# Kernel tuning notes

Measured on AMD Instinct MI355X. Metric: run time of the kernel, lower is better.

The kernel has to match this reference:

```python
import jax, jax.numpy as jnp
import numpy as np

N, F_IN, HID, H1, NG = 50000, 128, 64, 4, 512
E = 800000


def setup_inputs() -> dict:
    key = jax.random.key(0)
    ks = jax.random.split(key, 16)
    x = jax.random.normal(ks[0], (N, F_IN), dtype=jnp.float32)
    edge_index = jax.random.randint(ks[1], (2, E), 0, N, dtype=jnp.int64)
    batch = jnp.sort(jax.random.randint(ks[2], (N,), 0, NG, dtype=jnp.int64))
    s = 0.05
    W1 = jax.random.normal(ks[3], (F_IN, H1 * HID), dtype=jnp.float32) * s
    a_src1 = jax.random.normal(ks[4], (H1, HID), dtype=jnp.float32) * s
    a_dst1 = jax.random.normal(ks[5], (H1, HID), dtype=jnp.float32) * s
    b1 = jnp.zeros((H1 * HID,), dtype=jnp.float32)
    W2 = jax.random.normal(ks[6], (H1 * HID, HID), dtype=jnp.float32) * s
    a_src2 = jax.random.normal(ks[7], (1, HID), dtype=jnp.float32) * s
    a_dst2 = jax.random.normal(ks[8], (1, HID), dtype=jnp.float32) * s
    b2 = jnp.zeros((HID,), dtype=jnp.float32)
    Wc = jax.random.normal(ks[9], (HID, 2), dtype=jnp.float32) * s
    bc = jnp.zeros((2,), dtype=jnp.float32)
    return dict(x=x, edge_index=edge_index, batch=batch, W1=W1, a_src1=a_src1,
                a_dst1=a_dst1, b1=b1, W2=W2, a_src2=a_src2, a_dst2=a_dst2,
                b2=b2, Wc=Wc, bc=bc)


def gat_layer(x, W, a_src, a_dst, bias, src, dst, n):
    # PyG GATConv: h = x @ W per head; e_ij = LeakyReLU(a_src.h_j + a_dst.h_i),
    # softmax over incoming edges of each dst node, then scatter-add aggregate.
    H, D = a_src.shape
    h = (x @ W).reshape(n, H, D)                       # [N,H,D]
    asrc = jnp.einsum('nhd,hd->nh', h, a_src)          # [N,H]
    adst = jnp.einsum('nhd,hd->nh', h, a_dst)
    e = jax.nn.leaky_relu(asrc[src] + adst[dst], 0.2)  # [E,H]
    m = jax.lax.stop_gradient(jax.ops.segment_max(e, dst, num_segments=n))
    p = jnp.exp(e - m[dst])
    s = jax.ops.segment_sum(p, dst, num_segments=n)
    alpha = p / (s[dst] + 1e-16)                       # [E,H]
    out = jax.ops.segment_sum(alpha[:, :, None] * h[src], dst, num_segments=n)
    return out.reshape(n, H * D) + bias


def reference(x, edge_index, batch, W1, a_src1, a_dst1, b1, W2, a_src2, a_dst2, b2, Wc, bc):
    n = x.shape[0]
    loops = jnp.arange(n, dtype=edge_index.dtype)
    src = jnp.concatenate([edge_index[0], loops])  # add self-loops (PyG default)
    dst = jnp.concatenate([edge_index[1], loops])
    h = jax.nn.relu(gat_layer(x, W1, a_src1, a_dst1, b1, src, dst, n))
    h = jax.nn.relu(gat_layer(h, W2, a_src2, a_dst2, b2, src, dst, n))
    # global mean pool over graphs
    ng = NG
    sums = jax.ops.segment_sum(h, batch, num_segments=ng)
    cnts = jax.ops.segment_sum(jnp.ones((n,), h.dtype), batch, num_segments=ng)
    pooled = sums / jnp.maximum(cnts, 1.0)[:, None]
    logits = pooled @ Wc + bc
    return jax.nn.log_softmax(logits, axis=1)
```

## Files before the change

kernel.cpp:

```cpp
#include <hip/hip_runtime.h>
#include <hip/hip_bf16.h>
#include <cstddef>
#include <cstdint>

#define FIN   128
#define HID   64
#define H1    4
#define NGRAPH 512

typedef short bf16x8 __attribute__((ext_vector_type(8)));
typedef float f32x4  __attribute__((ext_vector_type(4)));

#if defined(__has_builtin)
#if __has_builtin(__builtin_amdgcn_cvt_f32_fp8) && __has_builtin(__builtin_amdgcn_cvt_pk_fp8_f32)
#define HAVE_HW_FP8 1
#endif
#endif

__device__ __forceinline__ float wave_reduce_sum(float v) {
  #pragma unroll
  for (int off = 32; off > 0; off >>= 1) v += __shfl_down(v, off, 64);
  return v;
}

__device__ __forceinline__ float leaky02(float x) {
  return x > 0.0f ? x : 0.2f * x;
}

__device__ __forceinline__ float bf2f(unsigned short u) {
  union { unsigned int i; float f; } v; v.i = ((unsigned int)u) << 16; return v.f;
}
__device__ __forceinline__ unsigned short f2bf(float f) {
  union { float f; unsigned int i; } v; v.f = f;
  unsigned int b = v.i;
  return (unsigned short)((b + 0x7FFFu + ((b >> 16) & 1u)) >> 16);
}

#ifndef HAVE_HW_FP8
__device__ __forceinline__ unsigned char f2fp8_1(float f) {
  unsigned int u = __float_as_uint(f);
  unsigned int s = u >> 31;
  u &= 0x7fffffffu;
  if (u > 0x43e00000u) u = 0x43e00000u;
  unsigned int b = u + (0x0007FFFFu + ((u >> 20) & 1u));
  int e = (int)(b >> 23) - 127;
  unsigned int m = (b >> 20) & 7u;
  unsigned char o;
  if (e < -9) o = 0;
  else if (e < -6) { int sh = -6 - e; o = (unsigned char)((8u | m) >> sh); }
  else if (e > 8) o = 0x7e;
  else o = (unsigned char)(((e + 7) << 3) | m);
  return o | (unsigned char)(s << 7);
}
__device__ __forceinline__ float fp8tof_1(unsigned char b) {
  unsigned int s = b >> 7, e = (b >> 3) & 15u, m = b & 7u;
  float v = (e == 0) ? (float)m * 0.001953125f
                     : (float)(8u + m) * __uint_as_float((117u + e) << 23);
  return s ? -v : v;
}
#endif

__device__ __forceinline__ unsigned char f2fp8(float f) {
#ifdef HAVE_HW_FP8
  return (unsigned char)(__builtin_amdgcn_cvt_pk_fp8_f32(f, f, 0u, false) & 0xffu);
#else
  return f2fp8_1(f);
#endif
}
__device__ __forceinline__ float fp8dec(unsigned int w, int i) {
#ifdef HAVE_HW_FP8
  switch (i) {
    case 0: return __builtin_amdgcn_cvt_f32_fp8(w, 0);
    case 1: return __builtin_amdgcn_cvt_f32_fp8(w, 1);
    case 2: return __builtin_amdgcn_cvt_f32_fp8(w, 2);
    default: return __builtin_amdgcn_cvt_f32_fp8(w, 3);
  }
#else
  return fp8tof_1((unsigned char)((w >> (8 * i)) & 0xffu));
#endif
}

__global__ void pre_kernel(const float* __restrict__ x, const float* __restrict__ W1,
                           const float* __restrict__ W2, unsigned short* __restrict__ xb,
                           unsigned short* __restrict__ W1T, unsigned short* __restrict__ W2T,
                           const int* __restrict__ batch, int* __restrict__ gstart,
                           int* __restrict__ gend, int nx8, int N) {
  int t = blockIdx.x * blockDim.x + threadIdx.x;
  if (t < nx8) {
    const float4* xp = (const float4*)x + (size_t)t * 2;
    float4 v0 = xp[0], v1 = xp[1];
    union { unsigned short u[8]; uint4 v; } r;
    r.u[0] = f2bf(v0.x); r.u[1] = f2bf(v0.y); r.u[2] = f2bf(v0.z); r.u[3] = f2bf(v0.w);
    r.u[4] = f2bf(v1.x); r.u[5] = f2bf(v1.y); r.u[6] = f2bf(v1.z); r.u[7] = f2bf(v1.w);
    *((uint4*)xb + t) = r.v;
  }
  if (t < N) {
    int g = batch[t];
    if (t == 0 || batch[t - 1] != g) gstart[g] = t;
    if (t == N - 1 || batch[t + 1] != g) gend[g] = t + 1;
  }
  int u = t - nx8;
  if (u >= 0 && u < 256 * 128) {
    int n = u >> 7, k = u & 127;
    W1T[u] = f2bf(W1[(size_t)k * 256 + n]);
  }
  u -= 256 * 128;
  if (u >= 0 && u < 64 * 256) {
    int n = u >> 8, k = u & 255;
    W2T[u] = f2bf(W2[(size_t)k * 64 + n]);
  }
}

__global__ __launch_bounds__(256)
void bhist_kernel(const int* __restrict__ dst, int* __restrict__ bucketCnt,
                  int E, int nbuck) {
  __shared__ int lh[256];
  int tid = threadIdx.x;
  lh[tid] = 0;
  __syncthreads();
  int stride = gridDim.x * 256;
  for (int i = blockIdx.x * 256 + tid; i < E; i += stride)
    atomicAdd(&lh[dst[i] >> 8], 1);
  __syncthreads();
  if (tid < nbuck && lh[tid] > 0) atomicAdd(&bucketCnt[tid], lh[tid]);
}

__global__ __launch_bounds__(256)
void bscan_kernel(const int* __restrict__ bucketCnt, int* __restrict__ bucketOff,
                  int* __restrict__ rowptrN, int nbuck) {
  __shared__ int lds[256];
  int t = threadIdx.x;
  int v = (t < nbuck) ? bucketCnt[t] : 0;
  lds[t] = v;
  __syncthreads();
  for (int off = 1; off < 256; off <<= 1) {
    int u = (t >= off) ? lds[t - off] : 0;
    __syncthreads();
    lds[t] += u;
    __syncthreads();
  }
  if (t < nbuck) bucketOff[t] = lds[t] - v;
  if (t == 255) { bucketOff[nbuck] = lds[255]; *rowptrN = lds[255]; }
}

#define P3K 16
__global__ __launch_bounds__(256)
void bpart_kernel(const int* __restrict__ src, const int* __restrict__ dst,
                  const int* __restrict__ bucketOff, int* __restrict__ bucketFill,
                  unsigned int* __restrict__ bucketBuf, int E, int nbuck) {
  __shared__ int lhist[256];
  __shared__ int lbase[256];
  __shared__ int lboff[256];
  int tid = threadIdx.x;
  if (tid < nbuck) lboff[tid] = bucketOff[tid];
  int chunk = 256 * P3K;
  for (int start = blockIdx.x * chunk; start < E; start += gridDim.x * chunk) {
    lhist[tid] = 0;
    __syncthreads();
    int mybuck[P3K]; unsigned int mypack[P3K]; int myrank[P3K];
    #pragma unroll
    for (int k = 0; k < P3K; k++) {
      int i = start + k * 256 + tid;
      if (i < E) {
        int d = dst[i];
        int b = d >> 8;
        mybuck[k] = b;
        mypack[k] = (unsigned int)src[i] | ((unsigned int)(d & 255) << 16);
        myrank[k] = atomicAdd(&lhist[b], 1);
      } else mybuck[k] = -1;
    }
    __syncthreads();
    if (tid < nbuck) lbase[tid] = (lhist[tid] > 0) ? atomicAdd(&bucketFill[tid], lhist[tid]) : 0;
    __syncthreads();
    #pragma unroll
    for (int k = 0; k < P3K; k++) {
      if (mybuck[k] >= 0) {
        int b = mybuck[k];
        bucketBuf[lboff[b] + lbase[b] + myrank[k]] = mypack[k];
      }
    }
    __syncthreads();
  }
}

__global__ __launch_bounds__(256)
void bbuild_kernel(const unsigned int* __restrict__ bucketBuf, const int* __restrict__ bucketOff,
                   int* __restrict__ rowptr, unsigned short* __restrict__ csr, int N) {
  __shared__ int ldeg[256];
  __shared__ int lscan[256];
  __shared__ int lfill[256];
  int b = blockIdx.x;
  int tid = threadIdx.x;
  int r0 = bucketOff[b], r1 = bucketOff[b + 1];
  int nb0 = b << 8;
  ldeg[tid] = 0;
  __syncthreads();
  for (int j = r0 + tid; j < r1; j += 256)
    atomicAdd(&ldeg[bucketBuf[j] >> 16], 1);
  __syncthreads();
  int v = ldeg[tid];
  lscan[tid] = v;
  __syncthreads();
  for (int off = 1; off < 256; off <<= 1) {
    int u = (tid >= off) ? lscan[tid - off] : 0;
    __syncthreads();
    lscan[tid] += u;
    __syncthreads();
  }
  int excl = lscan[tid] - v;
  lfill[tid] = excl;
  if (nb0 + tid < N) rowptr[nb0 + tid] = r0 + excl;
  __syncthreads();
  for (int j = r0 + tid; j < r1; j += 256) {
    unsigned int p = bucketBuf[j];
    int pos = r0 + atomicAdd(&lfill[p >> 16], 1);
    csr[pos] = (unsigned short)(p & 0xffffu);
  }
}

__global__ __launch_bounds__(256)
void gemm1_kernel(const unsigned short* __restrict__ Xb, const unsigned short* __restrict__ W1T,
                  unsigned char* __restrict__ h1f8,
                  const float* __restrict__ a_src, const float* __restrict__ a_dst,
                  float* __restrict__ asv, float* __restrict__ adv, int N) {
  __shared__ unsigned short As[64][136];
  __shared__ unsigned short Bs[256][40];
  int t = threadIdx.x;
  int w = t >> 6, lane = t & 63;
  int quad = lane >> 4, l16 = lane & 15;
  int blockRow = blockIdx.x * 64;

  {
    int node = t >> 2, kp = (t & 3) * 32;
    int gn = blockRow + node; if (gn >= N) gn = N - 1;
    const unsigned short* xp = Xb + (size_t)gn * 128 + kp;
    #pragma unroll
    for (int i = 0; i < 4; i++) {
      uint4 v = *(const uint4*)(xp + i * 8);
      *(uint4*)&As[node][kp + i * 8] = v;
    }
  }

  f32x4 acc[4][4];
  #pragma unroll
  for (int i = 0; i < 4; i++)
    #pragma unroll
    for (int j = 0; j < 4; j++) acc[i][j] = (f32x4){0.f, 0.f, 0.f, 0.f};

  for (int kc = 0; kc < FIN; kc += 32) {
    {
      const unsigned short* wp = W1T + (size_t)t * 128 + kc;
      #pragma unroll
      for (int i = 0; i < 4; i++) {
        uint4 v = *(const uint4*)(wp + i * 8);
        *(uint4*)&Bs[t][i * 8] = v;
      }
    }
    __syncthreads();
    bf16x8 af[4], bfr[4];
    #pragma unroll
    for (int mt = 0; mt < 4; mt++)
      af[mt] = *(const bf16x8*)&As[mt * 16 + l16][kc + quad * 8];
    #pragma unroll
    for (int nt = 0; nt < 4; nt++)
      bfr[nt] = *(const bf16x8*)&Bs[w * 64 + nt * 16 + l16][quad * 8];
    #pragma unroll
    for (int mt = 0; mt < 4; mt++)
      #pragma unroll
      for (int nt = 0; nt < 4; nt++)
        acc[mt][nt] = __builtin_amdgcn_mfma_f32_16x16x32_bf16(af[mt], bfr[nt], acc[mt][nt], 0, 0, 0);
    __syncthreads();
  }

  float a_s[4], a_d[4];
  #pragma unroll
  for (int nt = 0; nt < 4; nt++) {
    a_s[nt] = a_src[w * 64 + nt * 16 + l16];
    a_d[nt] = a_dst[w * 64 + nt * 16 + l16];
  }
  #pragma unroll
  for (int mt = 0; mt < 4; mt++) {
    #pragma unroll
    for (int reg = 0; reg < 4; reg++) {
      int node = blockRow + mt * 16 + quad * 4 + reg;
      bool ok = node < N;
      float ps = 0.0f, pd = 0.0f;
      #pragma unroll
      for (int nt = 0; nt < 4; nt++) {
        float v = acc[mt][nt][reg];
        ps = fmaf(v, a_s[nt], ps);
        pd = fmaf(v, a_d[nt], pd);
        if (ok) h1f8[(size_t)node * 256 + w * 64 + nt * 16 + l16] = f2fp8(v);
      }
      #pragma unroll
      for (int off = 8; off > 0; off >>= 1) {
        ps += __shfl_xor(ps, off, 16);
        pd += __shfl_xor(pd, off, 16);
      }
      if (l16 == 0 && ok) {
        asv[(size_t)node * 4 + w] = ps;
        adv[(size_t)node * 4 + w] = pd;
      }
    }
  }
}

__global__ __launch_bounds__(256)
void gemm2_kernel(const unsigned short* __restrict__ out1b, const unsigned short* __restrict__ W2T,
                  unsigned char* __restrict__ h2f8,
                  const float* __restrict__ a_src, const float* __restrict__ a_dst,
                  float* __restrict__ asv, float* __restrict__ adv, int N) {
  __shared__ unsigned short As[64][40];
  __shared__ unsigned short Bs[64][40];
  int t = threadIdx.x;
  int w = t >> 6, lane = t & 63;
  int quad = lane >> 4, l16 = lane & 15;
  int blockRow = blockIdx.x * 64;

  f32x4 acc[4];
  #pragma unroll
  for (int j = 0; j < 4; j++) acc[j] = (f32x4){0.f, 0.f, 0.f, 0.f};

  int nodeS = t >> 2, koff = (t & 3) * 8;
  int gnS = blockRow + nodeS; if (gnS >= N) gnS = N - 1;

  for (int kc = 0; kc < 256; kc += 32) {
    {
      uint4 va = *(const uint4*)(out1b + (size_t)gnS * 256 + kc + koff);
      *(uint4*)&As[nodeS][koff] = va;
      uint4 vb = *(const uint4*)(W2T + (size_t)nodeS * 256 + kc + koff);
      *(uint4*)&Bs[nodeS][koff] = vb;
    }
    __syncthreads();
    bf16x8 af = *(const bf16x8*)&As[w * 16 + l16][quad * 8];
    #pragma unroll
    for (int nt = 0; nt < 4; nt++) {
      bf16x8 bfr = *(const bf16x8*)&Bs[nt * 16 + l16][quad * 8];
      acc[nt] = __builtin_amdgcn_mfma_f32_16x16x32_bf16(af, bfr, acc[nt], 0, 0, 0);
    }
    __syncthreads();
  }

  float a_s[4], a_d[4];
  #pragma unroll
  for (int nt = 0; nt < 4; nt++) {
    a_s[nt] = a_src[nt * 16 + l16];
    a_d[nt] = a_dst[nt * 16 + l16];
  }
  #pragma unroll
  for (int reg = 0; reg < 4; reg++) {
    int node = blockRow + w * 16 + quad * 4 + reg;
    bool ok = node < N;
    float ps = 0.0f, pd = 0.0f;
    #pragma unroll
    for (int nt = 0; nt < 4; nt++) {
      float v = acc[nt][reg];
      ps = fmaf(v, a_s[nt], ps);
      pd = fmaf(v, a_d[nt], pd);
      if (ok) h2f8[(size_t)node * 64 + nt * 16 + l16] = f2fp8(v);
    }
    #pragma unroll
    for (int off = 8; off > 0; off >>= 1) {
      ps += __shfl_xor(ps, off, 16);
      pd += __shfl_xor(pd, off, 16);
    }
    if (l16 == 0 && ok) { asv[node] = ps; adv[node] = pd; }
  }
}

__global__ __launch_bounds__(256)
void agg1_kernel(const unsigned char* __restrict__ h1f8, const int* __restrict__ rowptr,
                 const unsigned short* __restrict__ csr, const float* __restrict__ asv,
                 const float* __restrict__ adv, const float* __restrict__ b1,
                 unsigned short* __restrict__ out1b, int N) {
  __shared__ int   sbuf[4][64];
  __shared__ float ebuf[4][4][68];
  int wv   = threadIdx.x >> 6;
  int lane = threadIdx.x & 63;
  int n = blockIdx.x * 4 + wv;
  if (n >= N) return;
  int r0 = rowptr[n], r1 = rowptr[n + 1];
  float4 ad = *(const float4*)(adv + (size_t)n * 4);
  float4 asn = *(const float4*)(asv + (size_t)n * 4);
  int hsel = lane >> 4;

  float es0 = leaky02(asn.x + ad.x);
  float es1 = leaky02(asn.y + ad.y);
  float es2 = leaky02(asn.z + ad.z);
  float es3 = leaky02(asn.w + ad.w);
  float esel  = hsel == 0 ? es0 : (hsel == 1 ? es1 : (hsel == 2 ? es2 : es3));
  float msel  = esel;
  float ssum = 0.0f;
  float a0 = 0, a1 = 0, a2 = 0, a3 = 0;

  for (int base = r0; base < r1; base += 64) {
    int j = base + lane;
    int cnt = min(64, r1 - base);
    float e0 = -1e30f, e1 = -1e30f, e2 = -1e30f, e3 = -1e30f;
    if (j < r1) {
      int s = csr[j];
      float4 as = *(const float4*)(asv + (size_t)s * 4);
      sbuf[wv][lane] = s;
      e0 = leaky02(as.x + ad.x);
      e1 = leaky02(as.y + ad.y);
      e2 = leaky02(as.z + ad.z);
      e3 = leaky02(as.w + ad.w);
      ebuf[wv][0][lane] = e0;
      ebuf[wv][1][lane] = e1;
      ebuf[wv][2][lane] = e2;
      ebuf[wv][3][lane] = e3;
    }
    __threadfence_block();
    #pragma unroll
    for (int off = 32; off > 0; off >>= 1) {
      e0 = fmaxf(e0, __shfl_xor(e0, off, 64));
      e1 = fmaxf(e1, __shfl_xor(e1, off, 64));
      e2 = fmaxf(e2, __shfl_xor(e2, off, 64));
      e3 = fmaxf(e3, __shfl_xor(e3, off, 64));
    }
    float csel = hsel == 0 ? e0 : (hsel == 1 ? e1 : (hsel == 2 ? e2 : e3));
    float mnew = fmaxf(msel, csel);
    float scl = __expf(msel - mnew);
    ssum *= scl; a0 *= scl; a1 *= scl; a2 *= scl; a3 *= scl;
    msel = mnew;

    int c = 0;
    for (; c + 4 <= cnt; c += 4) {
      int4 sv = *(const int4*)&sbuf[wv][c];
      int sc0 = __builtin_amdgcn_readfirstlane(sv.x);
      int sc1 = __builtin_amdgcn_readfirstlane(sv.y);
      int sc2 = __builtin_amdgcn_readfirstlane(sv.z);
      int sc3 = __builtin_amdgcn_readfirstlane(sv.w);
      unsigned int hw0 = *((const unsigned int*)(h1f8 + ((size_t)sc0 << 8)) + lane);
      unsigned int hw1 = *((const unsigned int*)(h1f8 + ((size_t)sc1 << 8)) + lane);
      unsigned int hw2 = *((const unsigned int*)(h1f8 + ((size_t)sc2 << 8)) + lane);
      unsigned int hw3 = *((const unsigned int*)(h1f8 + ((size_t)sc3 << 8)) + lane);
      float4 ev = *(const float4*)&ebuf[wv][hsel][c];
      float p0 = __expf(ev.x - msel);
      float p1 = __expf(ev.y - msel);
      float p2 = __expf(ev.z - msel);
      float p3 = __expf(ev.w - msel);
      ssum += (p0 + p1) + (p2 + p3);
      a0 = fmaf(p0, fp8dec(hw0, 0), a0);
      a1 = fmaf(p0, fp8dec(hw0, 1), a1);
      a2 = fmaf(p0, fp8dec(hw0, 2), a2);
      a3 = fmaf(p0, fp8dec(hw0, 3), a3);
      a0 = fmaf(p1, fp8dec(hw1, 0), a0);
      a1 = fmaf(p1, fp8dec(hw1, 1), a1);
      a2 = fmaf(p1, fp8dec(hw1, 2), a2);
      a3 = fmaf(p1, fp8dec(hw1, 3), a3);
      a0 = fmaf(p2, fp8dec(hw2, 0), a0);
      a1 = fmaf(p2, fp8dec(hw2, 1), a1);
      a2 = fmaf(p2, fp8dec(hw2, 2), a2);
      a3 = fmaf(p2, fp8dec(hw2, 3), a3);
      a0 = fmaf(p3, fp8dec(hw3, 0), a0);
      a1 = fmaf(p3, fp8dec(hw3, 1), a1);
      a2 = fmaf(p3, fp8dec(hw3, 2), a2);
      a3 = fmaf(p3, fp8dec(hw3, 3), a3);
    }
    for (; c < cnt; c++) {
      int sc = __builtin_amdgcn_readfirstlane(sbuf[wv][c]);
      float ec = ebuf[wv][hsel][c];
      float psel = __expf(ec - msel);
      ssum += psel;
      unsigned int hw = *((const unsigned int*)(h1f8 + ((size_t)sc << 8)) + lane);
      a0 = fmaf(psel, fp8dec(hw, 0), a0);
      a1 = fmaf(psel, fp8dec(hw, 1), a1);
      a2 = fmaf(psel, fp8dec(hw, 2), a2);
      a3 = fmaf(psel, fp8dec(hw, 3), a3);
    }
    __threadfence_block();
  }

  {
    float psel = __expf(esel - msel);
    ssum += psel;
    unsigned int hw = *((const unsigned int*)(h1f8 + ((size_t)n << 8)) + lane);
    a0 = fmaf(psel, fp8dec(hw, 0), a0);
    a1 = fmaf(psel, fp8dec(hw, 1), a1);
    a2 = fmaf(psel, fp8dec(hw, 2), a2);
    a3 = fmaf(psel, fp8dec(hw, 3), a3);
  }

  float inv = 1.0f / (ssum + 1e-16f);
  int d0 = lane * 4;
  float4 bv = *(const float4*)(b1 + d0);
  float v0 = a0 * inv + bv.x;
  float v1 = a1 * inv + bv.y;
  float v2 = a2 * inv + bv.z;
  float v3 = a3 * inv + bv.w;
  ushort4 o;
  o.x = f2bf(v0 > 0 ? v0 : 0.0f);
  o.y = f2bf(v1 > 0 ? v1 : 0.0f);
  o.z = f2bf(v2 > 0 ? v2 : 0.0f);
  o.w = f2bf(v3 > 0 ? v3 : 0.0f);
  *(ushort4*)(out1b + (size_t)n * 256 + d0) = o;
}

__global__ __launch_bounds__(256)
void agg2_kernel(const unsigned char* __restrict__ h2f8, const int* __restrict__ rowptr,
                 const unsigned short* __restrict__ csr, const float* __restrict__ asv,
                 const float* __restrict__ adv, const float* __restrict__ b2,
                 float* __restrict__ h2out, int N) {
  __shared__ int   sbuf[4][64];
  __shared__ float ebuf[4][64];
  int wv   = threadIdx.x >> 6;
  int lane = threadIdx.x & 63;
  int quad = lane >> 4, l16 = lane & 15;
  int n = blockIdx.x * 4 + wv;
  if (n >= N) return;
  int r0 = rowptr[n], r1 = rowptr[n + 1];
  float ad = adv[n];
  float eself = leaky02(asv[n] + ad);
  float m = eself;
  float ssum = 0.0f;
  float a0 = 0, a1 = 0, a2 = 0, a3 = 0;

  for (int base = r0; base < r1; base += 64) {
    int j = base + lane;
    int cnt = min(64, r1 - base);
    float e = -1e30f;
    if (j < r1) {
      int s = csr[j];
      sbuf[wv][lane] = s;
      e = leaky02(asv[s] + ad);
      ebuf[wv][lane] = e;
    }
    __threadfence_block();
    float cm = e;
    #pragma unroll
    for (int off = 32; off > 0; off >>= 1)
      cm = fmaxf(cm, __shfl_xor(cm, off, 64));
    float mnew = fmaxf(m, cm);
    float scl = __expf(m - mnew);
    ssum *= scl; a0 *= scl; a1 *= scl; a2 *= scl; a3 *= scl;
    m = mnew;

    int c = 0;
    for (; c + 4 <= cnt; c += 4) {
      int sc = sbuf[wv][c + quad];
      float p = __expf(ebuf[wv][c + quad] - m);
      ssum += p;
      unsigned int hw = *((const unsigned int*)(h2f8 + ((size_t)sc << 6)) + l16);
      a0 = fmaf(p, fp8dec(hw, 0), a0);
      a1 = fmaf(p, fp8dec(hw, 1), a1);
      a2 = fmaf(p, fp8dec(hw, 2), a2);
      a3 = fmaf(p, fp8dec(hw, 3), a3);
    }
    int rem = cnt - c;
    if (quad < rem) {
      int sc = sbuf[wv][c + quad];
      float p = __expf(ebuf[wv][c + quad] - m);
      ssum += p;
      unsigned int hw = *((const unsigned int*)(h2f8 + ((size_t)sc << 6)) + l16);
      a0 = fmaf(p, fp8dec(hw, 0), a0);
      a1 = fmaf(p, fp8dec(hw, 1), a1);
      a2 = fmaf(p, fp8dec(hw, 2), a2);
      a3 = fmaf(p, fp8dec(hw, 3), a3);
    }
    __threadfence_block();
  }

  #pragma unroll
  for (int off = 16; off <= 32; off <<= 1) {
    ssum += __shfl_xor(ssum, off, 64);
    a0 += __shfl_xor(a0, off, 64);
    a1 += __shfl_xor(a1, off, 64);
    a2 += __shfl_xor(a2, off, 64);
    a3 += __shfl_xor(a3, off, 64);
  }

  {
    float p = __expf(eself - m);
    ssum += p;
    unsigned int hw = *((const unsigned int*)(h2f8 + ((size_t)n << 6)) + l16);
    a0 = fmaf(p, fp8dec(hw, 0), a0);
    a1 = fmaf(p, fp8dec(hw, 1), a1);
    a2 = fmaf(p, fp8dec(hw, 2), a2);
    a3 = fmaf(p, fp8dec(hw, 3), a3);
  }

  if (quad == 0) {
    float inv = 1.0f / (ssum + 1e-16f);
    float4 bv = *(const float4*)(b2 + l16 * 4);
    float4 o;
    float v0 = a0 * inv + bv.x;
    float v1 = a1 * inv + bv.y;
    float v2 = a2 * inv + bv.z;
    float v3 = a3 * inv + bv.w;
    o.x = v0 > 0 ? v0 : 0.0f;
    o.y = v1 > 0 ? v1 : 0.0f;
    o.z = v2 > 0 ? v2 : 0.0f;
    o.w = v3 > 0 ? v3 : 0.0f;
    *(float4*)(h2out + (size_t)n * 64 + l16 * 4) = o;
  }
}

__global__ __launch_bounds__(256)
void pool_kernel(const float* __restrict__ h2, const int* __restrict__ gstart,
                 const int* __restrict__ gend, const float* __restrict__ Wc,
                 const float* __restrict__ bc, float* __restrict__ out) {
  int g = blockIdx.x;
  int w = threadIdx.x >> 6, lane = threadIdx.x & 63;
  int s = gstart[g], e = gend[g];
  float acc = 0.0f;
  for (int n = s + w; n < e; n += 4) acc += h2[(size_t)n * 64 + lane];
  __shared__ float red[4][64];
  red[w][lane] = acc;
  __syncthreads();
  if (w == 0) {
    float v = red[0][lane] + red[1][lane] + red[2][lane] + red[3][lane];
    float pooled = (e > s) ? v / (float)(e - s) : 0.0f;
    float l0 = wave_reduce_sum(pooled * Wc[lane * 2 + 0]);
    float l1 = wave_reduce_sum(pooled * Wc[lane * 2 + 1]);
    if (lane == 0) {
      l0 += bc[0]; l1 += bc[1];
      float mx = fmaxf(l0, l1);
      float lse = mx + logf(__expf(l0 - mx) + __expf(l1 - mx));
      out[g * 2 + 0] = l0 - lse;
      out[g * 2 + 1] = l1 - lse;
    }
  }
}

extern "C" void kernel_launch(void* const* d_in, const int* in_sizes, int n_in,
                              void* d_out, int out_size, void* d_ws, size_t ws_size,
                              hipStream_t stream) {
  const float* x      = (const float*)d_in[0];
  const int*   ei     = (const int*)d_in[1];
  const int*   batch  = (const int*)d_in[2];
  const float* W1     = (const float*)d_in[3];
  const float* a_src1 = (const float*)d_in[4];
  const float* a_dst1 = (const float*)d_in[5];
  const float* b1     = (const float*)d_in[6];
  const float* W2     = (const float*)d_in[7];
  const float* a_src2 = (const float*)d_in[8];
  const float* a_dst2 = (const float*)d_in[9];
  const float* b2     = (const float*)d_in[10];
  const float* Wc     = (const float*)d_in[11];
  const float* bc     = (const float*)d_in[12];
  float* out = (float*)d_out;

  const int N = in_sizes[0] / FIN;
  const int E = in_sizes[1] / 2;
  const int* srcArr = ei;
  const int* dstArr = ei + E;
  const int nbuck = (N + 255) >> 8;

  char* base = (char*)d_ws;
  size_t off = 0;
  auto alloc = [&](size_t bytes) -> void* {
    void* p = base + off;
    off = (off + bytes + 255) & ~(size_t)255;
    return p;
  };
  unsigned short* xb   = (unsigned short*)alloc((size_t)N * 128 * 2);
  unsigned short* W1T  = (unsigned short*)alloc((size_t)256 * 128 * 2);
  unsigned short* W2T  = (unsigned short*)alloc((size_t)64 * 256 * 2);
  unsigned char*  h1f8 = (unsigned char*)alloc((size_t)N * 256);
  unsigned short* out1b= (unsigned short*)alloc((size_t)N * 256 * 2);
  unsigned char*  h2f8 = (unsigned char*)alloc((size_t)N * 64);
  float* h2    = (float*)alloc((size_t)N * 64 * 4);
  float* asv1  = (float*)alloc((size_t)N * 4 * 4);
  float* adv1  = (float*)alloc((size_t)N * 4 * 4);
  float* asv2  = (float*)alloc((size_t)N * 4);
  float* adv2  = (float*)alloc((size_t)N * 4);
  int*   bucketCnt = (int*)alloc(256 * 4);
  int*   bucketFill= (int*)alloc(256 * 4);
  int*   gstart= (int*)alloc(NGRAPH * 4);
  int*   gend  = (int*)alloc(NGRAPH * 4);
  size_t zspan = (size_t)((char*)gend + NGRAPH * 4 - (char*)bucketCnt);
  int*   bucketOff = (int*)alloc(257 * 4);
  int*   rowptr= (int*)alloc(((size_t)N + 1) * 4);
  unsigned int* bucketBuf = (unsigned int*)alloc((size_t)E * 4);
  unsigned short* csr = (unsigned short*)alloc((size_t)E * 2);
  (void)ws_size; (void)n_in; (void)out_size;

  int gridWv = (N + 3) / 4;
  int gridG  = (N + 63) / 64;
  int nx8    = N * 128 / 8;
  int wtot   = 256 * 128 + 64 * 256;
  int gridP  = (nx8 + wtot + 255) / 256;
  int gridP3 = (E + 256 * P3K - 1) / (256 * P3K);

  hipMemsetAsync(bucketCnt, 0, zspan, stream);
  pre_kernel<<<gridP, 256, 0, stream>>>(x, W1, W2, xb, W1T, W2T, batch, gstart, gend, nx8, N);
  bhist_kernel<<<512, 256, 0, stream>>>(dstArr, bucketCnt, E, nbuck);
  bscan_kernel<<<1, 256, 0, stream>>>(bucketCnt, bucketOff, rowptr + N, nbuck);
  bpart_kernel<<<gridP3, 256, 0, stream>>>(srcArr, dstArr, bucketOff, bucketFill, bucketBuf, E, nbuck);
  bbuild_kernel<<<nbuck, 256, 0, stream>>>(bucketBuf, bucketOff, rowptr, csr, N);

  gemm1_kernel<<<gridG, 256, 0, stream>>>(xb, W1T, h1f8, a_src1, a_dst1, asv1, adv1, N);
  agg1_kernel<<<gridWv, 256, 0, stream>>>(h1f8, rowptr, csr, asv1, adv1, b1, out1b, N);

  gemm2_kernel<<<gridG, 256, 0, stream>>>(out1b, W2T, h2f8, a_src2, a_dst2, asv2, adv2, N);
  agg2_kernel<<<gridWv, 256, 0, stream>>>(h2f8, rowptr, csr, asv2, adv2, b2, h2, N);

  pool_kernel<<<NGRAPH, 256, 0, stream>>>(h2, gstart, gend, Wc, bc, out);
}
```

Measured before the change: 248.6 us.

## Fuse CSR build stages, convert x inline in gemm1, precompute edge probabilities

After: 296.8 us. 19.4% more time.

```diff
diff --git a/kernel.cpp b/kernel.cpp
--- a/kernel.cpp
+++ b/kernel.cpp
@@ -7,6 +7,7 @@
 #define HID   64
 #define H1    4
 #define NGRAPH 512
+#define BCAP  8192
 
 typedef short bf16x8 __attribute__((ext_vector_type(8)));
 typedef float f32x4  __attribute__((ext_vector_type(4)));
@@ -27,9 +28,6 @@
   return x > 0.0f ? x : 0.2f * x;
 }
 
-__device__ __forceinline__ float bf2f(unsigned short u) {
-  union { unsigned int i; float f; } v; v.i = ((unsigned int)u) << 16; return v.f;
-}
 __device__ __forceinline__ unsigned short f2bf(float f) {
   union { float f; unsigned int i; } v; v.f = f;
   unsigned int b = v.i;
@@ -80,26 +78,24 @@
 #endif
 }
 
-__global__ void pre_kernel(const float* __restrict__ x, const float* __restrict__ W1,
-                           const float* __restrict__ W2, unsigned short* __restrict__ xb,
-                           unsigned short* __restrict__ W1T, unsigned short* __restrict__ W2T,
-                           const int* __restrict__ batch, int* __restrict__ gstart,
-                           int* __restrict__ gend, int nx8, int N) {
-  int t = blockIdx.x * blockDim.x + threadIdx.x;
-  if (t < nx8) {
-    const float4* xp = (const float4*)x + (size_t)t * 2;
-    float4 v0 = xp[0], v1 = xp[1];
-    union { unsigned short u[8]; uint4 v; } r;
-    r.u[0] = f2bf(v0.x); r.u[1] = f2bf(v0.y); r.u[2] = f2bf(v0.z); r.u[3] = f2bf(v0.w);
-    r.u[4] = f2bf(v1.x); r.u[5] = f2bf(v1.y); r.u[6] = f2bf(v1.z); r.u[7] = f2bf(v1.w);
-    *((uint4*)xb + t) = r.v;
-  }
+__global__ __launch_bounds__(256)
+void pre_kernel(const float* __restrict__ W1, const float* __restrict__ W2,
+                unsigned short* __restrict__ W1T, unsigned short* __restrict__ W2T,
+                const int* __restrict__ dst, int* __restrict__ bucketCnt,
+                const int* __restrict__ batch, int* __restrict__ gstart,
+                int* __restrict__ gend, int E, int N, int nbuck) {
+  __shared__ int lh[256];
+  int tid = threadIdx.x;
+  lh[tid] = 0;
+  __syncthreads();
+  int t = blockIdx.x * 256 + tid;
+  if (t < E) atomicAdd(&lh[dst[t] >> 8], 1);
   if (t < N) {
     int g = batch[t];
     if (t == 0 || batch[t - 1] != g) gstart[g] = t;
     if (t == N - 1 || batch[t + 1] != g) gend[g] = t + 1;
   }
-  int u = t - nx8;
+  int u = t - E;
   if (u >= 0 && u < 256 * 128) {
     int n = u >> 7, k = u & 127;
     W1T[u] = f2bf(W1[(size_t)k * 256 + n]);
@@ -109,50 +105,18 @@
     int n = u >> 8, k = u & 255;
     W2T[u] = f2bf(W2[(size_t)k * 64 + n]);
   }
-}
-
-__global__ __launch_bounds__(256)
-void bhist_kernel(const int* __restrict__ dst, int* __restrict__ bucketCnt,
-                  int E, int nbuck) {
-  __shared__ int lh[256];
-  int tid = threadIdx.x;
-  lh[tid] = 0;
-  __syncthreads();
-  int stride = gridDim.x * 256;
-  for (int i = blockIdx.x * 256 + tid; i < E; i += stride)
-    atomicAdd(&lh[dst[i] >> 8], 1);
   __syncthreads();
   if (tid < nbuck && lh[tid] > 0) atomicAdd(&bucketCnt[tid], lh[tid]);
 }
 
-__global__ __launch_bounds__(256)
-void bscan_kernel(const int* __restrict__ bucketCnt, int* __restrict__ bucketOff,
-                  int* __restrict__ rowptrN, int nbuck) {
-  __shared__ int lds[256];
-  int t = threadIdx.x;
-  int v = (t < nbuck) ? bucketCnt[t] : 0;
-  lds[t] = v;
-  __syncthreads();
-  for (int off = 1; off < 256; off <<= 1) {
-    int u = (t >= off) ? lds[t - off] : 0;
-    __syncthreads();
-    lds[t] += u;
-    __syncthreads();
-  }
-  if (t < nbuck) bucketOff[t] = lds[t] - v;
-  if (t == 255) { bucketOff[nbuck] = lds[255]; *rowptrN = lds[255]; }
-}
-
 #define P3K 16
 __global__ __launch_bounds__(256)
 void bpart_kernel(const int* __restrict__ src, const int* __restrict__ dst,
-                  const int* __restrict__ bucketOff, int* __restrict__ bucketFill,
-                  unsigned int* __restrict__ bucketBuf, int E, int nbuck) {
+                  int* __restrict__ bucketFill, unsigned int* __restrict__ bucketBuf,
+                  int E, int nbuck) {
   __shared__ int lhist[256];
   __shared__ int lbase[256];
-  __shared__ int lboff[256];
   int tid = threadIdx.x;
-  if (tid < nbuck) lboff[tid] = bucketOff[tid];
   int chunk = 256 * P3K;
   for (int start = blockIdx.x * chunk; start < E; start += gridDim.x * chunk) {
     lhist[tid] = 0;
@@ -176,7 +140,8 @@
     for (int k = 0; k < P3K; k++) {
       if (mybuck[k] >= 0) {
         int b = mybuck[k];
-        bucketBuf[lboff[b] + lbase[b] + myrank[k]] = mypack[k];
+        int pos = lbase[b] + myrank[k];
+        if (pos < BCAP) bucketBuf[((size_t)b << 13) + pos] = mypack[k];
       }
     }
     __syncthreads();
@@ -184,19 +149,21 @@
 }
 
 __global__ __launch_bounds__(256)
-void bbuild_kernel(const unsigned int* __restrict__ bucketBuf, const int* __restrict__ bucketOff,
-                   int* __restrict__ rowptr, unsigned short* __restrict__ csr, int N) {
+void bbuild_kernel(const unsigned int* __restrict__ bucketBuf, const int* __restrict__ bucketCnt,
+                   int* __restrict__ rowstart, int* __restrict__ rowend,
+                   unsigned short* __restrict__ csr, int N) {
   __shared__ int ldeg[256];
   __shared__ int lscan[256];
   __shared__ int lfill[256];
   int b = blockIdx.x;
   int tid = threadIdx.x;
-  int r0 = bucketOff[b], r1 = bucketOff[b + 1];
+  int r0 = b << 13;
+  int cnt = bucketCnt[b]; if (cnt > BCAP) cnt = BCAP;
   int nb0 = b << 8;
   ldeg[tid] = 0;
   __syncthreads();
-  for (int j = r0 + tid; j < r1; j += 256)
-    atomicAdd(&ldeg[bucketBuf[j] >> 16], 1);
+  for (int j = tid; j < cnt; j += 256)
+    atomicAdd(&ldeg[bucketBuf[r0 + j] >> 16], 1);
   __syncthreads();
   int v = ldeg[tid];
   lscan[tid] = v;
@@ -209,17 +176,20 @@
   }
   int excl = lscan[tid] - v;
   lfill[tid] = excl;
-  if (nb0 + tid < N) rowptr[nb0 + tid] = r0 + excl;
+  if (nb0 + tid < N) {
+    rowstart[nb0 + tid] = r0 + excl;
+    rowend[nb0 + tid]   = r0 + excl + v;
+  }
   __syncthreads();
-  for (int j = r0 + tid; j < r1; j += 256) {
-    unsigned int p = bucketBuf[j];
+  for (int j = tid; j < cnt; j += 256) {
+    unsigned int p = bucketBuf[r0 + j];
     int pos = r0 + atomicAdd(&lfill[p >> 16], 1);
     csr[pos] = (unsigned short)(p & 0xffffu);
   }
 }
 
 __global__ __launch_bounds__(256)
-void gemm1_kernel(const unsigned short* __restrict__ Xb, const unsigned short* __restrict__ W1T,
+void gemm1_kernel(const float* __restrict__ X, const unsigned short* __restrict__ W1T,
                   unsigned char* __restrict__ h1f8,
                   const float* __restrict__ a_src, const float* __restrict__ a_dst,
                   float* __restrict__ asv, float* __restrict__ adv, int N) {
@@ -233,11 +203,14 @@
   {
     int node = t >> 2, kp = (t & 3) * 32;
     int gn = blockRow + node; if (gn >= N) gn = N - 1;
-    const unsigned short* xp = Xb + (size_t)gn * 128 + kp;
+    const float4* xp = (const float4*)(X + (size_t)gn * 128 + kp);
     #pragma unroll
     for (int i = 0; i < 4; i++) {
-      uint4 v = *(const uint4*)(xp + i * 8);
-      *(uint4*)&As[node][kp + i * 8] = v;
+      float4 va = xp[2 * i], vb = xp[2 * i + 1];
+      union { unsigned short u[8]; uint4 v; } r;
+      r.u[0] = f2bf(va.x); r.u[1] = f2bf(va.y); r.u[2] = f2bf(va.z); r.u[3] = f2bf(va.w);
+      r.u[4] = f2bf(vb.x); r.u[5] = f2bf(vb.y); r.u[6] = f2bf(vb.z); r.u[7] = f2bf(vb.w);
+      *(uint4*)&As[node][kp + i * 8] = r.v;
     }
   }
 
@@ -369,17 +342,17 @@
 }
 
 __global__ __launch_bounds__(256)
-void agg1_kernel(const unsigned char* __restrict__ h1f8, const int* __restrict__ rowptr,
-                 const unsigned short* __restrict__ csr, const float* __restrict__ asv,
-                 const float* __restrict__ adv, const float* __restrict__ b1,
-                 unsigned short* __restrict__ out1b, int N) {
+void agg1_kernel(const unsigned char* __restrict__ h1f8, const int* __restrict__ rowstart,
+                 const int* __restrict__ rowend, const unsigned short* __restrict__ csr,
+                 const float* __restrict__ asv, const float* __restrict__ adv,
+                 const float* __restrict__ b1, unsigned short* __restrict__ out1b, int N) {
   __shared__ int   sbuf[4][64];
-  __shared__ float ebuf[4][4][68];
+  __shared__ float pbuf[4][4][68];
   int wv   = threadIdx.x >> 6;
   int lane = threadIdx.x & 63;
   int n = blockIdx.x * 4 + wv;
   if (n >= N) return;
-  int r0 = rowptr[n], r1 = rowptr[n + 1];
+  int r0 = rowstart[n], r1 = rowend[n];
   float4 ad = *(const float4*)(adv + (size_t)n * 4);
   float4 asn = *(const float4*)(asv + (size_t)n * 4);
   int hsel = lane >> 4;
@@ -388,8 +361,9 @@
   float es1 = leaky02(asn.y + ad.y);
   float es2 = leaky02(asn.z + ad.z);
   float es3 = leaky02(asn.w + ad.w);
-  float esel  = hsel == 0 ? es0 : (hsel == 1 ? es1 : (hsel == 2 ? es2 : es3));
-  float msel  = esel;
+  float esel = hsel == 0 ? es0 : (hsel == 1 ? es1 : (hsel == 2 ? es2 : es3));
+  float m0r = es0, m1r = es1, m2r = es2, m3r = es3;
+  float mselr = esel;
   float ssum = 0.0f;
   float a0 = 0, a1 = 0, a2 = 0, a3 = 0;
 
@@ -405,12 +379,8 @@
       e1 = leaky02(as.y + ad.y);
       e2 = leaky02(as.z + ad.z);
       e3 = leaky02(as.w + ad.w);
-      ebuf[wv][0][lane] = e0;
-      ebuf[wv][1][lane] = e1;
-      ebuf[wv][2][lane] = e2;
-      ebuf[wv][3][lane] = e3;
-    }
-    __threadfence_block();
+    }
+    float f0 = e0, f1 = e1, f2 = e2, f3 = e3;
     #pragma unroll
     for (int off = 32; off > 0; off >>= 1) {
       e0 = fmaxf(e0, __shfl_xor(e0, off, 64));
@@ -418,11 +388,30 @@
       e2 = fmaxf(e2, __shfl_xor(e2, off, 64));
       e3 = fmaxf(e3, __shfl_xor(e3, off, 64));
     }
-    float csel = hsel == 0 ? e0 : (hsel == 1 ? e1 : (hsel == 2 ? e2 : e3));
-    float mnew = fmaxf(msel, csel);
-    float scl = __expf(msel - mnew);
+    float m0n = fmaxf(m0r, e0), m1n = fmaxf(m1r, e1);
+    float m2n = fmaxf(m2r, e2), m3n = fmaxf(m3r, e3);
+    float mseln = hsel == 0 ? m0n : (hsel == 1 ? m1n : (hsel == 2 ? m2n : m3n));
+    float scl = __expf(mselr - mseln);
     ssum *= scl; a0 *= scl; a1 *= scl; a2 *= scl; a3 *= scl;
-    msel = mnew;
+    m0r = m0n; m1r = m1n; m2r = m2n; m3r = m3n; mselr = mseln;
+
+    float p0 = __expf(f0 - m0n);
+    float p1 = __expf(f1 - m1n);
+    float p2 = __expf(f2 - m2n);
+    float p3 = __expf(f3 - m3n);
+    pbuf[wv][0][lane] = p0;
+    pbuf[wv][1][lane] = p1;
+    pbuf[wv][2][lane] = p2;
+    pbuf[wv][3][lane] = p3;
+    #pragma unroll
+    for (int off = 32; off > 0; off >>= 1) {
+      p0 += __shfl_xor(p0, off, 64);
+      p1 += __shfl_xor(p1, off, 64);
+      p2 += __shfl_xor(p2, off, 64);
+      p3 += __shfl_xor(p3, off, 64);
+    }
+    ssum += hsel == 0 ? p0 : (hsel == 1 ? p1 : (hsel == 2 ? p2 : p3));
+    __threadfence_block();
 
     int c = 0;
     for (; c + 4 <= cnt; c += 4) {
@@ -435,34 +424,27 @@
       unsigned int hw1 = *((const unsigned int*)(h1f8 + ((size_t)sc1 << 8)) + lane);
       unsigned int hw2 = *((const unsigned int*)(h1f8 + ((size_t)sc2 << 8)) + lane);
       unsigned int hw3 = *((const unsigned int*)(h1f8 + ((size_t)sc3 << 8)) + lane);
-      float4 ev = *(const float4*)&ebuf[wv][hsel][c];
-      float p0 = __expf(ev.x - msel);
-      float p1 = __expf(ev.y - msel);
-      float p2 = __expf(ev.z - msel);
-      float p3 = __expf(ev.w - msel);
-      ssum += (p0 + p1) + (p2 + p3);
-      a0 = fmaf(p0, fp8dec(hw0, 0), a0);
-      a1 = fmaf(p0, fp8dec(hw0, 1), a1);
-      a2 = fmaf(p0, fp8dec(hw0, 2), a2);
-      a3 = fmaf(p0, fp8dec(hw0, 3), a3);
-      a0 = fmaf(p1, fp8dec(hw1, 0), a0);
-      a1 = fmaf(p1, fp8dec(hw1, 1), a1);
-      a2 = fmaf(p1, fp8dec(hw1, 2), a2);
-      a3 = fmaf(p1, fp8dec(hw1, 3), a3);
-      a0 = fmaf(p2, fp8dec(hw2, 0), a0);
-      a1 = fmaf(p2, fp8dec(hw2, 1), a1);
-      a2 = fmaf(p2, fp8dec(hw2, 2), a2);
-      a3 = fmaf(p2, fp8dec(hw2, 3), a3);
-      a0 = fmaf(p3, fp8dec(hw3, 0), a0);
-      a1 = fmaf(p3, fp8dec(hw3, 1), a1);
-      a2 = fmaf(p3, fp8dec(hw3, 2), a2);
-      a3 = fmaf(p3, fp8dec(hw3, 3), a3);
+      float4 pv = *(const float4*)&pbuf[wv][hsel][c];
+      a0 = fmaf(pv.x, fp8dec(hw0, 0), a0);
+      a1 = fmaf(pv.x, fp8dec(hw0, 1), a1);
+      a2 = fmaf(pv.x, fp8dec(hw0, 2), a2);
+      a3 = fmaf(pv.x, fp8dec(hw0, 3), a3);
+      a0 = fmaf(pv.y, fp8dec(hw1, 0), a0);
+      a1 = fmaf(pv.y, fp8dec(hw1, 1), a1);
+      a2 = fmaf(pv.y, fp8dec(hw1, 2), a2);
+      a3 = fmaf(pv.y, fp8dec(hw1, 3), a3);
+      a0 = fmaf(pv.z, fp8dec(hw2, 0), a0);
+      a1 = fmaf(pv.z, fp8dec(hw2, 1), a1);
+      a2 = fmaf(pv.z, fp8dec(hw2, 2), a2);
+      a3 = fmaf(pv.z, fp8dec(hw2, 3), a3);
+      a0 = fmaf(pv.w, fp8dec(hw3, 0), a0);
+      a1 = fmaf(pv.w, fp8dec(hw3, 1), a1);
+      a2 = fmaf(pv.w, fp8dec(hw3, 2), a2);
+      a3 = fmaf(pv.w, fp8dec(hw3, 3), a3);
     }
     for (; c < cnt; c++) {
       int sc = __builtin_amdgcn_readfirstlane(sbuf[wv][c]);
-      float ec = ebuf[wv][hsel][c];
-      float psel = __expf(ec - msel);
-      ssum += psel;
+      float psel = pbuf[wv][hsel][c];
       unsigned int hw = *((const unsigned int*)(h1f8 + ((size_t)sc << 8)) + lane);
       a0 = fmaf(psel, fp8dec(hw, 0), a0);
       a1 = fmaf(psel, fp8dec(hw, 1), a1);
@@ -473,7 +455,7 @@
   }
 
   {
-    float psel = __expf(esel - msel);
+    float psel = __expf(esel - mselr);
     ssum += psel;
     unsigned int hw = *((const unsigned int*)(h1f8 + ((size_t)n << 8)) + lane);
     a0 = fmaf(psel, fp8dec(hw, 0), a0);
@@ -498,18 +480,18 @@
 }
 
 __global__ __launch_bounds__(256)
-void agg2_kernel(const unsigned char* __restrict__ h2f8, const int* __restrict__ rowptr,
-                 const unsigned short* __restrict__ csr, const float* __restrict__ asv,
-                 const float* __restrict__ adv, const float* __restrict__ b2,
-                 float* __restrict__ h2out, int N) {
+void agg2_kernel(const unsigned char* __restrict__ h2f8, const int* __restrict__ rowstart,
+                 const int* __restrict__ rowend, const unsigned short* __restrict__ csr,
+                 const float* __restrict__ asv, const float* __restrict__ adv,
+                 const float* __restrict__ b2, float* __restrict__ h2out, int N) {
   __shared__ int   sbuf[4][64];
-  __shared__ float ebuf[4][64];
+  __shared__ float pbuf[4][64];
   int wv   = threadIdx.x >> 6;
   int lane = threadIdx.x & 63;
   int quad = lane >> 4, l16 = lane & 15;
   int n = blockIdx.x * 4 + wv;
   if (n >= N) return;
-  int r0 = rowptr[n], r1 = rowptr[n + 1];
+  int r0 = rowstart[n], r1 = rowend[n];
   float ad = adv[n];
   float eself = leaky02(asv[n] + ad);
   float m = eself;
@@ -524,46 +506,65 @@
       int s = csr[j];
       sbuf[wv][lane] = s;
       e = leaky02(asv[s] + ad);
-      ebuf[wv][lane] = e;
-    }
-    __threadfence_block();
-    float cm = e;
+    }
+    float f = e;
     #pragma unroll
     for (int off = 32; off > 0; off >>= 1)
-      cm = fmaxf(cm, __shfl_xor(cm, off, 64));
-    float mnew = fmaxf(m, cm);
+      e = fmaxf(e, __shfl_xor(e, off, 64));
+    float mnew = fmaxf(m, e);
     float scl = __expf(m - mnew);
     ssum *= scl; a0 *= scl; a1 *= scl; a2 *= scl; a3 *= scl;
     m = mnew;
 
+    float p = __expf(f - mnew);
+    pbuf[wv][lane] = p;
+    #pragma unroll
+    for (int off = 32; off > 0; off >>= 1)
+      p += __shfl_xor(p, off, 64);
+    ssum += p;
+    __threadfence_block();
+
     int c = 0;
+    for (; c + 8 <= cnt; c += 8) {
+      int scA = sbuf[wv][c + quad];
+      int scB = sbuf[wv][c + 4 + quad];
+      float pA = pbuf[wv][c + quad];
+      float pB = pbuf[wv][c + 4 + quad];
+      unsigned int hwA = *((const unsigned int*)(h2f8 + ((size_t)scA << 6)) + l16);
+      unsigned int hwB = *((const unsigned int*)(h2f8 + ((size_t)scB << 6)) + l16);
+      a0 = fmaf(pA, fp8dec(hwA, 0), a0);
+      a1 = fmaf(pA, fp8dec(hwA, 1), a1);
+      a2 = fmaf(pA, fp8dec(hwA, 2), a2);
+      a3 = fmaf(pA, fp8dec(hwA, 3), a3);
+      a0 = fmaf(pB, fp8dec(hwB, 0), a0);
+      a1 = fmaf(pB, fp8dec(hwB, 1), a1);
+      a2 = fmaf(pB, fp8dec(hwB, 2), a2);
+      a3 = fmaf(pB, fp8dec(hwB, 3), a3);
+    }
     for (; c + 4 <= cnt; c += 4) {
       int sc = sbuf[wv][c + quad];
-      float p = __expf(ebuf[wv][c + quad] - m);
-      ssum += p;
+      float p1 = pbuf[wv][c + quad];
       unsigned int hw = *((const unsigned int*)(h2f8 + ((size_t)sc << 6)) + l16);
-      a0 = fmaf(p, fp8dec(hw, 0), a0);
-      a1 = fmaf(p, fp8dec(hw, 1), a1);
-      a2 = fmaf(p, fp8dec(hw, 2), a2);
-      a3 = fmaf(p, fp8dec(hw, 3), a3);
+      a0 = fmaf(p1, fp8dec(hw, 0), a0);
+      a1 = fmaf(p1, fp8dec(hw, 1), a1);
+      a2 = fmaf(p1, fp8dec(hw, 2), a2);
+      a3 = fmaf(p1, fp8dec(hw, 3), a3);
     }
     int rem = cnt - c;
     if (quad < rem) {
       int sc = sbuf[wv][c + quad];
-      float p = __expf(ebuf[wv][c + quad] - m);
-      ssum += p;
+      float p1 = pbuf[wv][c + quad];
       unsigned int hw = *((const unsigned int*)(h2f8 + ((size_t)sc << 6)) + l16);
-      a0 = fmaf(p, fp8dec(hw, 0), a0);
-      a1 = fmaf(p, fp8dec(hw, 1), a1);
-      a2 = fmaf(p, fp8dec(hw, 2), a2);
-      a3 = fmaf(p, fp8dec(hw, 3), a3);
+      a0 = fmaf(p1, fp8dec(hw, 0), a0);
+      a1 = fmaf(p1, fp8dec(hw, 1), a1);
+      a2 = fmaf(p1, fp8dec(hw, 2), a2);
+      a3 = fmaf(p1, fp8dec(hw, 3), a3);
     }
     __threadfence_block();
   }
 
   #pragma unroll
   for (int off = 16; off <= 32; off <<= 1) {
-    ssum += __shfl_xor(ssum, off, 64);
     a0 += __shfl_xor(a0, off, 64);
     a1 += __shfl_xor(a1, off, 64);
     a2 += __shfl_xor(a2, off, 64);
@@ -654,7 +655,6 @@
     off = (off + bytes + 255) & ~(size_t)255;
     return p;
   };
-  unsigned short* xb   = (unsigned short*)alloc((size_t)N * 128 * 2);
   unsigned short* W1T  = (unsigned short*)alloc((size_t)256 * 128 * 2);
   unsigned short* W2T  = (unsigned short*)alloc((size_t)64 * 256 * 2);
   unsigned char*  h1f8 = (unsigned char*)alloc((size_t)N * 256);
@@ -670,31 +670,29 @@
   int*   gstart= (int*)alloc(NGRAPH * 4);
   int*   gend  = (int*)alloc(NGRAPH * 4);
   size_t zspan = (size_t)((char*)gend + NGRAPH * 4 - (char*)bucketCnt);
-  int*   bucketOff = (int*)alloc(257 * 4);
-  int*   rowptr= (int*)alloc(((size_t)N + 1) * 4);
-  unsigned int* bucketBuf = (unsigned int*)alloc((size_t)E * 4);
-  unsigned short* csr = (unsigned short*)alloc((size_t)E * 2);
+  int*   rowstart = (int*)alloc((size_t)N * 4);
+  int*   rowend   = (int*)alloc((size_t)N * 4);
+  unsigned int* bucketBuf = (unsigned int*)alloc((size_t)nbuck * BCAP * 4);
+  unsigned short* csr = (unsigned short*)alloc((size_t)nbuck * BCAP * 2);
   (void)ws_size; (void)n_in; (void)out_size;
 
   int gridWv = (N + 3) / 4;
   int gridG  = (N + 63) / 64;
-  int nx8    = N * 128 / 8;
   int wtot   = 256 * 128 + 64 * 256;
-  int gridP  = (nx8 + wtot + 255) / 256;
+  int gridP  = (E + wtot + 255) / 256;
   int gridP3 = (E + 256 * P3K - 1) / (256 * P3K);
 
   hipMemsetAsync(bucketCnt, 0, zspan, stream);
-  pre_kernel<<<gridP, 256, 0, stream>>>(x, W1, W2, xb, W1T, W2T, batch, gstart, gend, nx8, N);
-  bhist_kernel<<<512, 256, 0, stream>>>(dstArr, bucketCnt, E, nbuck);
-  bscan_kernel<<<1, 256, 0, stream>>>(bucketCnt, bucketOff, rowptr + N, nbuck);
-  bpart_kernel<<<gridP3, 256, 0, stream>>>(srcArr, dstArr, bucketOff, bucketFill, bucketBuf, E, nbuck);
-  bbuild_kernel<<<nbuck, 256, 0, stream>>>(bucketBuf, bucketOff, rowptr, csr, N);
-
-  gemm1_kernel<<<gridG, 256, 0, stream>>>(xb, W1T, h1f8, a_src1, a_dst1, asv1, adv1, N);
-  agg1_kernel<<<gridWv, 256, 0, stream>>>(h1f8, rowptr, csr, asv1, adv1, b1, out1b, N);
+  pre_kernel<<<gridP, 256, 0, stream>>>(W1, W2, W1T, W2T, dstArr, bucketCnt,
+                                        batch, gstart, gend, E, N, nbuck);
+  bpart_kernel<<<gridP3, 256, 0, stream>>>(srcArr, dstArr, bucketFill, bucketBuf, E, nbuck);
+  bbuild_kernel<<<nbuck, 256, 0, stream>>>(bucketBuf, bucketCnt, rowstart, rowend, csr, N);
+
+  gemm1_kernel<<<gridG, 256, 0, stream>>>(x, W1T, h1f8, a_src1, a_dst1, asv1, adv1, N);
+  agg1_kernel<<<gridWv, 256, 0, stream>>>(h1f8, rowstart, rowend, csr, asv1, adv1, b1, out1b, N);
 
   gemm2_kernel<<<gridG, 256, 0, stream>>>(out1b, W2T, h2f8, a_src2, a_dst2, asv2, adv2, N);
-  agg2_kernel<<<gridWv, 256, 0, stream>>>(h2f8, rowptr, csr, asv2, adv2, b2, h2, N);
+  agg2_kernel<<<gridWv, 256, 0, stream>>>(h2f8, rowstart, rowend, csr, asv2, adv2, b2, h2, N);
 
   pool_kernel<<<NGRAPH, 256, 0, stream>>>(h2, gstart, gend, Wc, bc, out);
 }
```
